# Performance work log

Hardware: AMD Instinct MI355X
Metric: run time of the kernel (lower is better)

The kernel has to match this reference:

```python
import jax, jax.numpy as jnp
import numpy as np

EMB = 1024
HEADS = 16
HEAD_DIM = EMB // HEADS


def setup_inputs() -> dict:
    key = jax.random.key(0)
    ks = jax.random.split(key, 12)
    B, S = 4, 2048
    scale = 1.0 / np.sqrt(EMB)
    inp = {
        'values': jax.random.normal(ks[0], (B, S, EMB), jnp.float32),
        'keys': jax.random.normal(ks[1], (B, S, EMB), jnp.float32),
        'query': jax.random.normal(ks[2], (B, S, EMB), jnp.float32),
        'Wv': jax.random.normal(ks[3], (EMB, EMB), jnp.float32) * scale,
        'bv': jnp.zeros((EMB,), jnp.float32),
        'Wk': jax.random.normal(ks[4], (EMB, EMB), jnp.float32) * scale,
        'bk': jnp.zeros((EMB,), jnp.float32),
        'Wq': jax.random.normal(ks[5], (EMB, EMB), jnp.float32) * scale,
        'bq': jnp.zeros((EMB,), jnp.float32),
        'Wo': jax.random.normal(ks[6], (EMB, EMB), jnp.float32) * scale,
        'bo': jnp.zeros((EMB,), jnp.float32),
    }
    return inp


def reference(values, keys, query, Wv, bv, Wk, bk, Wq, bq, Wo, bo):
    B, S, _ = values.shape
    # Linear projections (torch Linear: x @ W.T + b)
    v = values @ Wv.T + bv
    k = keys @ Wk.T + bk
    q = query @ Wq.T + bq
    # Reshape to (B, S, H, D) -- NOTE: original does NOT transpose heads,
    # so attention is computed across the HEAD axis per position.
    v = v.reshape(B, S, HEADS, HEAD_DIM)
    k = k.reshape(B, S, HEADS, HEAD_DIM)
    q = q.reshape(B, S, HEADS, HEAD_DIM)
    # (B,S,H,D) @ (B,S,D,H) -> (B,S,H,H) head-head scores
    scores = jnp.einsum('bshd,bsgd->bshg', q, k) * (HEAD_DIM ** -0.5)
    attn = jax.nn.softmax(scores, axis=-1)
    # (B,S,H,H) @ (B,S,H,D) -> (B,S,H,D)
    out = jnp.einsum('bshg,bsgd->bshd', attn, v)
    out = out.reshape(B, S, EMB)
    return out @ Wo.T + bo
```

## Files before the change

### kernel.cpp

```cpp
#include <hip/hip_runtime.h>
#include <stdint.h>

#define EMB 1024

typedef unsigned short u16;
typedef unsigned int u32;
typedef __attribute__((ext_vector_type(8))) unsigned short u16x8;
typedef __attribute__((ext_vector_type(8))) __bf16 bf16x8;
typedef __attribute__((ext_vector_type(4))) float f32x4;

__device__ __forceinline__ u16 f2bf(float f) {
  union { float f; uint32_t u; } x; x.f = f;
  uint32_t u = x.u;
  u += 0x7fff + ((u >> 16) & 1u);
  return (u16)(u >> 16);
}

__device__ __forceinline__ bf16x8 cvt8(float4 a, float4 b) {
  bf16x8 r;
  r[0] = (__bf16)a.x; r[1] = (__bf16)a.y; r[2] = (__bf16)a.z; r[3] = (__bf16)a.w;
  r[4] = (__bf16)b.x; r[5] = (__bf16)b.y; r[6] = (__bf16)b.z; r[7] = (__bf16)b.w;
  return r;
}

__device__ __forceinline__ void gl16(const u16* g, u16* l) {
  __builtin_amdgcn_global_load_lds(
      (const __attribute__((address_space(1))) void*)g,
      (__attribute__((address_space(3))) void*)l, 16, 0, 0);
}

__device__ __forceinline__ int xcd_logical(int orig, int nwg) {
  return (orig & 7) * (nwg >> 3) + (orig >> 3);
}

__global__ __launch_bounds__(256) void cvtw_kernel(
    const float* __restrict__ s0, u16* __restrict__ d0,
    const float* __restrict__ s1, u16* __restrict__ d1,
    const float* __restrict__ s2, u16* __restrict__ d2,
    const float* __restrict__ s3, u16* __restrict__ d3)
{
  const float* s; u16* d;
  switch (blockIdx.y) {
    case 0:  s = s0; d = d0; break;
    case 1:  s = s1; d = d1; break;
    case 2:  s = s2; d = d2; break;
    default: s = s3; d = d3; break;
  }
  const size_t i = (size_t)blockIdx.x * 256 + threadIdx.x;
  const float4* f = (const float4*)(s + i * 8);
  const float4 lo = f[0], hi = f[1];
  *(bf16x8*)(d + i * 8) = cvt8(lo, hi);
}

__global__ __launch_bounds__(256, 4) void qkv_fused_kernel(
    const float* __restrict__ Vx, const float* __restrict__ Kx,
    const float* __restrict__ Qx, const u16* __restrict__ Wb,
    const float* __restrict__ Bv, const float* __restrict__ Bk,
    const float* __restrict__ Bq,
    u16* __restrict__ cv, u16* __restrict__ ck, u16* __restrict__ cq,
    int N, int K, int M)
{
  __shared__ __attribute__((aligned(16))) u16 Al[2][128 * 32];
  __shared__ __attribute__((aligned(16))) u16 Bl[3][128 * 32];

  const int nwg = (N >> 7) * (M >> 7) * 3;
  const int logical = xcd_logical(blockIdx.x, nwg);
  const int per_z = (N >> 7) * (M >> 7);
  const int z = logical / per_z;
  const int rem = logical - z * per_z;
  const int nbx = N >> 7;
  const int by = rem / nbx, bx = rem - by * nbx;

  const float* X; const u16* W; const float* Bias; u16* C;
  switch (z) {
    case 0:  X = Vx; W = Wb;                   Bias = Bv; C = cv; break;
    case 1:  X = Kx; W = Wb + EMB * EMB;       Bias = Bk; C = ck; break;
    default: X = Qx; W = Wb + 2 * EMB * EMB;   Bias = Bq; C = cq; break;
  }

  const int tid  = threadIdx.x;
  const int lane = tid & 63;
  const int w    = tid >> 6;
  const int wm = w >> 1, wn = w & 1;
  const int r16 = lane & 15, quad = lane >> 4;
  const int bm = by * 128, bn = bx * 128;

  const int NSTEP = K >> 5;
  const int SM = NSTEP - 1;

  const int s0 = tid, s1 = tid + 256;
  const int r0 = s0 >> 2, c0 = s0 & 3;
  const int r1 = s1 >> 2, c1 = s1 & 3;
  const int lA0 = r0 * 32 + ((c0 ^ ((r0 >> 1) & 3)) * 8);
  const int lA1 = r1 * 32 + ((c1 ^ ((r1 >> 1) & 3)) * 8);
  const size_t xo0 = (size_t)(bm + r0) * K + c0 * 8;
  const size_t xo1 = (size_t)(bm + r1) * K + c1 * 8;

  const int bs0 = w * 64 + lane, bs1 = bs0 + 256;
  const int br0 = bs0 >> 2, bc0 = ((bs0 & 3) ^ ((br0 >> 1) & 3)) * 8;
  const int br1 = bs1 >> 2, bc1 = ((bs1 & 3) ^ ((br1 >> 1) & 3)) * 8;
  const u16* srcB0 = W + (size_t)(bn + br0) * K + bc0;
  const u16* srcB1 = W + (size_t)(bn + br1) * K + bc1;
  const int dB0o = (w * 64) * 8, dB1o = dB0o + 256 * 8;

  const int swz = (quad ^ ((r16 >> 1) & 3)) * 8;
  int offA[4], offB[4];
#pragma unroll
  for (int t = 0; t < 4; t++) {
    offA[t] = (wm * 64 + t * 16 + r16) * 32 + swz;
    offB[t] = (wn * 64 + t * 16 + r16) * 32 + swz;
  }

  f32x4 acc[4][4];
#pragma unroll
  for (int i = 0; i < 4; i++)
#pragma unroll
    for (int j = 0; j < 4; j++)
      acc[i][j] = f32x4{0.f, 0.f, 0.f, 0.f};

  float4 xa0 = *(const float4*)(X + xo0), xa1 = *(const float4*)(X + xo0 + 4);
  float4 xb0 = *(const float4*)(X + xo1), xb1 = *(const float4*)(X + xo1 + 4);
  gl16(srcB0, &Bl[0][dB0o]);
  gl16(srcB1, &Bl[0][dB1o]);
  gl16(srcB0 + 32, &Bl[1][dB0o]);
  gl16(srcB1 + 32, &Bl[1][dB1o]);
  *(bf16x8*)&Al[0][lA0] = cvt8(xa0, xa1);
  *(bf16x8*)&Al[0][lA1] = cvt8(xb0, xb1);
  xa0 = *(const float4*)(X + xo0 + 32); xa1 = *(const float4*)(X + xo0 + 36);
  xb0 = *(const float4*)(X + xo1 + 32); xb1 = *(const float4*)(X + xo1 + 36);
  asm volatile("s_waitcnt vmcnt(0) lgkmcnt(0)\n\ts_barrier" ::: "memory");

  int brd = 0;
  for (int it = 0; it < NSTEP; ++it) {
    const int acur = it & 1, anxt = acur ^ 1;
    const int bwr = (brd == 0) ? 2 : brd - 1;
    const int kn2 = ((it + 2) & SM) << 5;

    gl16(srcB0 + kn2, &Bl[bwr][dB0o]);
    gl16(srcB1 + kn2, &Bl[bwr][dB1o]);
    *(bf16x8*)&Al[anxt][lA0] = cvt8(xa0, xa1);
    *(bf16x8*)&Al[anxt][lA1] = cvt8(xb0, xb1);
    xa0 = *(const float4*)(X + xo0 + kn2); xa1 = *(const float4*)(X + xo0 + kn2 + 4);
    xb0 = *(const float4*)(X + xo1 + kn2); xb1 = *(const float4*)(X + xo1 + kn2 + 4);

    bf16x8 a[4], b[4];
#pragma unroll
    for (int t = 0; t < 4; t++) a[t] = *(const bf16x8*)&Al[acur][offA[t]];
#pragma unroll
    for (int t = 0; t < 4; t++) b[t] = *(const bf16x8*)&Bl[brd][offB[t]];

#pragma unroll
    for (int tm = 0; tm < 4; tm++)
#pragma unroll
      for (int tn = 0; tn < 4; tn++)
        acc[tm][tn] = __builtin_amdgcn_mfma_f32_16x16x32_bf16(a[tm], b[tn], acc[tm][tn], 0, 0, 0);

    asm volatile("s_waitcnt vmcnt(6) lgkmcnt(0)\n\ts_barrier" ::: "memory");
    brd = (brd == 2) ? 0 : brd + 1;
  }

#pragma unroll
  for (int tn = 0; tn < 4; tn++) {
    const int col = bn + wn * 64 + tn * 16 + r16;
    const float bias = Bias[col];
#pragma unroll
    for (int tm = 0; tm < 4; tm++) {
      const int row0 = bm + wm * 64 + tm * 16 + quad * 4;
#pragma unroll
      for (int r = 0; r < 4; r++)
        C[(size_t)(row0 + r) * N + col] = f2bf(acc[tm][tn][r] + bias);
    }
  }
}

__global__ __launch_bounds__(256, 4) void out_gemm_kernel(
    const u16* __restrict__ X, const u16* __restrict__ W,
    const float* __restrict__ Bias, float* __restrict__ C, int N, int K, int M)
{
  __shared__ __attribute__((aligned(16))) u16 Al[3][128 * 32];
  __shared__ __attribute__((aligned(16))) u16 Bl[3][64 * 32];

  const int nwg = (N >> 6) * (M >> 7);
  const int logical = xcd_logical(blockIdx.x, nwg);
  const int nbx = N >> 6;
  const int by = logical / nbx, bx = logical - by * nbx;

  const int tid  = threadIdx.x;
  const int lane = tid & 63;
  const int w    = tid >> 6;
  const int wm = w >> 1, wn = w & 1;
  const int r16 = lane & 15, quad = lane >> 4;
  const int bm = by * 128, bn = bx * 64;

  const int NSTEP = K >> 5;
  const int SM = NSTEP - 1;

  const int sA0 = w * 64 + lane, sA1 = sA0 + 256;
  const int rA0 = sA0 >> 2, cA0 = ((sA0 & 3) ^ ((rA0 >> 1) & 3)) * 8;
  const int rA1 = sA1 >> 2, cA1 = ((sA1 & 3) ^ ((rA1 >> 1) & 3)) * 8;
  const u16* srcA0 = X + (size_t)(bm + rA0) * K + cA0;
  const u16* srcA1 = X + (size_t)(bm + rA1) * K + cA1;
  const int dA0o = (w * 64) * 8, dA1o = dA0o + 256 * 8;

  const int sB = w * 64 + lane;
  const int rB = sB >> 2, cB = ((sB & 3) ^ ((rB >> 1) & 3)) * 8;
  const u16* srcB = W + (size_t)(bn + rB) * K + cB;
  const int dBo = (w * 64) * 8;

  const int swz = (quad ^ ((r16 >> 1) & 3)) * 8;
  int offA[4], offB[2];
#pragma unroll
  for (int t = 0; t < 4; t++)
    offA[t] = (wm * 64 + t * 16 + r16) * 32 + swz;
#pragma unroll
  for (int t = 0; t < 2; t++)
    offB[t] = (wn * 32 + t * 16 + r16) * 32 + swz;

  f32x4 acc[4][2];
#pragma unroll
  for (int i = 0; i < 4; i++)
#pragma unroll
    for (int j = 0; j < 2; j++)
      acc[i][j] = f32x4{0.f, 0.f, 0.f, 0.f};

  gl16(srcA0, &Al[0][dA0o]);
  gl16(srcA1, &Al[0][dA1o]);
  gl16(srcB,  &Bl[0][dBo]);
  gl16(srcA0 + 32, &Al[1][dA0o]);
  gl16(srcA1 + 32, &Al[1][dA1o]);
  gl16(srcB  + 32, &Bl[1][dBo]);
  asm volatile("s_waitcnt vmcnt(0)\n\ts_barrier" ::: "memory");

  int rd = 0;
  for (int it = 0; it < NSTEP; ++it) {
    const int wr = (rd == 0) ? 2 : rd - 1;
    const int kn2 = ((it + 2) & SM) << 5;

    gl16(srcA0 + kn2, &Al[wr][dA0o]);
    gl16(srcA1 + kn2, &Al[wr][dA1o]);
    gl16(srcB  + kn2, &Bl[wr][dBo]);

    bf16x8 a[4], b[2];
#pragma unroll
    for (int t = 0; t < 4; t++) a[t] = *(const bf16x8*)&Al[rd][offA[t]];
#pragma unroll
    for (int t = 0; t < 2; t++) b[t] = *(const bf16x8*)&Bl[rd][offB[t]];

#pragma unroll
    for (int tm = 0; tm < 4; tm++)
#pragma unroll
      for (int tn = 0; tn < 2; tn++)
        acc[tm][tn] = __builtin_amdgcn_mfma_f32_16x16x32_bf16(a[tm], b[tn], acc[tm][tn], 0, 0, 0);

    asm volatile("s_waitcnt vmcnt(3)\n\ts_barrier" ::: "memory");
    rd = (rd == 2) ? 0 : rd + 1;
  }

#pragma unroll
  for (int tn = 0; tn < 2; tn++) {
    const int col = bn + wn * 32 + tn * 16 + r16;
    const float bias = Bias[col];
#pragma unroll
    for (int tm = 0; tm < 4; tm++) {
      const int row0 = bm + wm * 64 + tm * 16 + quad * 4;
#pragma unroll
      for (int r = 0; r < 4; r++)
        C[(size_t)(row0 + r) * N + col] = acc[tm][tn][r] + bias;
    }
  }
}

__global__ __launch_bounds__(256, 5) void attn_heads_kernel(
    const u16* __restrict__ Q, const u16* __restrict__ Km,
    const u16* __restrict__ V, u16* __restrict__ O)
{
  const int tid = threadIdx.x, lane = tid & 63, w = tid >> 6;
  const int r16 = lane & 15, quad = lane >> 4;
  const size_t base = ((size_t)blockIdx.x * 4 + w) * EMB;

  u16 vb[4][8];
  const bool vload = quad < 2;
#pragma unroll
  for (int c = 0; c < 4; c++)
#pragma unroll
    for (int j = 0; j < 8; j++)
      vb[c][j] = vload ? V[base + (quad * 8 + j) * 64 + c * 16 + r16] : (u16)0;

  const bf16x8 ak0 = *(const bf16x8*)&Km[base + r16 * 64 + quad * 8];
  const bf16x8 ak1 = *(const bf16x8*)&Km[base + r16 * 64 + 32 + quad * 8];
  const bf16x8 bq0 = *(const bf16x8*)&Q[base + r16 * 64 + quad * 8];
  const bf16x8 bq1 = *(const bf16x8*)&Q[base + r16 * 64 + 32 + quad * 8];

  f32x4 s = f32x4{0.f, 0.f, 0.f, 0.f};
  s = __builtin_amdgcn_mfma_f32_16x16x32_bf16(ak0, bq0, s, 0, 0, 0);
  s = __builtin_amdgcn_mfma_f32_16x16x32_bf16(ak1, bq1, s, 0, 0, 0);

  float sv[4];
#pragma unroll
  for (int r = 0; r < 4; r++) sv[r] = s[r] * 0.125f;
  float m = fmaxf(fmaxf(sv[0], sv[1]), fmaxf(sv[2], sv[3]));
  m = fmaxf(m, __shfl_xor(m, 16));
  m = fmaxf(m, __shfl_xor(m, 32));
  float e[4];
  float sum = 0.f;
#pragma unroll
  for (int r = 0; r < 4; r++) { e[r] = __expf(sv[r] - m); sum += e[r]; }
  sum += __shfl_xor(sum, 16);
  sum += __shfl_xor(sum, 32);
  const float rs = 1.0f / sum;

  union { __bf16 h[2]; u32 u; } wlo, whi;
  wlo.h[0] = (__bf16)(e[0] * rs); wlo.h[1] = (__bf16)(e[1] * rs);
  whi.h[0] = (__bf16)(e[2] * rs); whi.h[1] = (__bf16)(e[3] * rs);

  const int src0 = r16 + quad * 32;
  const int src1 = src0 + 16;
  u32 a0 = (u32)__shfl((int)wlo.u, src0, 64);
  u32 a1 = (u32)__shfl((int)whi.u, src0, 64);
  u32 a2 = (u32)__shfl((int)wlo.u, src1, 64);
  u32 a3 = (u32)__shfl((int)whi.u, src1, 64);
  if (quad >= 2) { a0 = 0; a1 = 0; a2 = 0; a3 = 0; }
  union { u32 u[4]; bf16x8 v; } pa;
  pa.u[0] = a0; pa.u[1] = a1; pa.u[2] = a2; pa.u[3] = a3;

#pragma unroll
  for (int c = 0; c < 4; c++) {
    union { u16 s[8]; bf16x8 v; } vbv;
#pragma unroll
    for (int j = 0; j < 8; j++) vbv.s[j] = vb[c][j];
    f32x4 o = f32x4{0.f, 0.f, 0.f, 0.f};
    o = __builtin_amdgcn_mfma_f32_16x16x32_bf16(pa.v, vbv.v, o, 0, 0, 0);
#pragma unroll
    for (int r = 0; r < 4; r++)
      O[base + (size_t)(quad * 4 + r) * 64 + c * 16 + r16] = f2bf(o[r]);
  }
}

extern "C" void kernel_launch(void* const* d_in, const int* in_sizes, int n_in,
                              void* d_out, int out_size, void* d_ws, size_t ws_size,
                              hipStream_t stream)
{
  const float* values = (const float*)d_in[0];
  const float* keys   = (const float*)d_in[1];
  const float* query  = (const float*)d_in[2];
  const float* Wv = (const float*)d_in[3];
  const float* bv = (const float*)d_in[4];
  const float* Wk = (const float*)d_in[5];
  const float* bk = (const float*)d_in[6];
  const float* Wq = (const float*)d_in[7];
  const float* bq = (const float*)d_in[8];
  const float* Wo = (const float*)d_in[9];
  const float* bo = (const float*)d_in[10];

  const int M = in_sizes[0] / EMB;
  const int N = EMB, K = EMB;

  u16* q    = (u16*)d_ws;
  u16* kbuf = q + (size_t)M * EMB;
  u16* v    = (u16*)d_out;
  u16* wb   = v + (size_t)M * EMB;
  u16* ao   = q;

  const size_t base_ws = (size_t)2 * M * EMB * sizeof(u16);
  const bool wo_in_ws = ws_size >= base_ws + (size_t)EMB * EMB * sizeof(u16);
  u16* wob = wo_in_ws ? kbuf + (size_t)M * EMB : kbuf;

  dim3 blk(256, 1, 1);
  dim3 cwg(EMB * EMB / 8 / 256, wo_in_ws ? 4 : 3, 1);

  hipLaunchKernelGGL(cvtw_kernel, cwg, blk, 0, stream,
                     Wv, wb, Wk, wb + EMB * EMB, Wq, wb + 2 * EMB * EMB, Wo, wob);
  hipLaunchKernelGGL(qkv_fused_kernel, dim3((N / 128) * (M / 128) * 3, 1, 1), blk, 0, stream,
                     values, keys, query, wb, bv, bk, bq, v, kbuf, q, N, K, M);
  hipLaunchKernelGGL(attn_heads_kernel, dim3(M / 4, 1, 1), blk, 0, stream,
                     q, kbuf, v, ao);
  if (!wo_in_ws)
    hipLaunchKernelGGL(cvtw_kernel, dim3(EMB * EMB / 8 / 256, 1, 1), blk, 0, stream,
                       Wo, wob, (const float*)nullptr, (u16*)nullptr,
                       (const float*)nullptr, (u16*)nullptr,
                       (const float*)nullptr, (u16*)nullptr);
  hipLaunchKernelGGL(out_gemm_kernel, dim3((N / 64) * (M / 128), 1, 1), blk, 0, stream,
                     ao, wob, bo, (float*)d_out, N, K, M);
}
```

Measured before the change: 276.3 us.

## Enlarge QKV projection GEMM tiles to 256x256 with 8 waves and phased MFMA pipeline

Replaces the 128x128 QKV GEMM kernel with a 256x256 tile, 512-thread (8 wave) kernel using BK=64 double-buffered LDS, a new XOR swizzle, and four interleaved MFMA phases with setprio and barriers between global-to-LDS stores. The larger tile is meant to cut redundant global reads of the fp32 activations and bf16 weights and raise arithmetic intensity per byte loaded. In exchange it uses 128 KB of LDS per block, gives one block per CU, and launches far fewer workgroups (384), which risks lower occupancy and poorer latency hiding.

```diff
diff --git a/kernel.cpp b/kernel.cpp
--- a/kernel.cpp
+++ b/kernel.cpp
@@ -52,7 +52,7 @@
   *(bf16x8*)(d + i * 8) = cvt8(lo, hi);
 }
 
-__global__ __launch_bounds__(256, 4) void qkv_fused_kernel(
+__global__ __launch_bounds__(512, 2) void qkv256_kernel(
     const float* __restrict__ Vx, const float* __restrict__ Kx,
     const float* __restrict__ Qx, const u16* __restrict__ Wb,
     const float* __restrict__ Bv, const float* __restrict__ Bk,
@@ -60,15 +60,15 @@
     u16* __restrict__ cv, u16* __restrict__ ck, u16* __restrict__ cq,
     int N, int K, int M)
 {
-  __shared__ __attribute__((aligned(16))) u16 Al[2][128 * 32];
-  __shared__ __attribute__((aligned(16))) u16 Bl[3][128 * 32];
-
-  const int nwg = (N >> 7) * (M >> 7) * 3;
+  __shared__ __attribute__((aligned(16))) u16 Al[2][256 * 64];
+  __shared__ __attribute__((aligned(16))) u16 Bl[2][256 * 64];
+
+  const int per_z = (M >> 8) * (N >> 8);
+  const int nwg = per_z * 3;
   const int logical = xcd_logical(blockIdx.x, nwg);
-  const int per_z = (N >> 7) * (M >> 7);
   const int z = logical / per_z;
   const int rem = logical - z * per_z;
-  const int nbx = N >> 7;
+  const int nbx = N >> 8;
   const int by = rem / nbx, bx = rem - by * nbx;
 
   const float* X; const u16* W; const float* Bias; u16* C;
@@ -81,91 +81,114 @@
   const int tid  = threadIdx.x;
   const int lane = tid & 63;
   const int w    = tid >> 6;
-  const int wm = w >> 1, wn = w & 1;
+  const int wm = w >> 2, wn = w & 3;
   const int r16 = lane & 15, quad = lane >> 4;
-  const int bm = by * 128, bn = bx * 128;
-
-  const int NSTEP = K >> 5;
-  const int SM = NSTEP - 1;
-
-  const int s0 = tid, s1 = tid + 256;
-  const int r0 = s0 >> 2, c0 = s0 & 3;
-  const int r1 = s1 >> 2, c1 = s1 & 3;
-  const int lA0 = r0 * 32 + ((c0 ^ ((r0 >> 1) & 3)) * 8);
-  const int lA1 = r1 * 32 + ((c1 ^ ((r1 >> 1) & 3)) * 8);
-  const size_t xo0 = (size_t)(bm + r0) * K + c0 * 8;
-  const size_t xo1 = (size_t)(bm + r1) * K + c1 * 8;
-
-  const int bs0 = w * 64 + lane, bs1 = bs0 + 256;
-  const int br0 = bs0 >> 2, bc0 = ((bs0 & 3) ^ ((br0 >> 1) & 3)) * 8;
-  const int br1 = bs1 >> 2, bc1 = ((bs1 & 3) ^ ((br1 >> 1) & 3)) * 8;
-  const u16* srcB0 = W + (size_t)(bn + br0) * K + bc0;
-  const u16* srcB1 = W + (size_t)(bn + br1) * K + bc1;
-  const int dB0o = (w * 64) * 8, dB1o = dB0o + 256 * 8;
-
-  const int swz = (quad ^ ((r16 >> 1) & 3)) * 8;
-  int offA[4], offB[4];
-#pragma unroll
-  for (int t = 0; t < 4; t++) {
-    offA[t] = (wm * 64 + t * 16 + r16) * 32 + swz;
-    offB[t] = (wn * 64 + t * 16 + r16) * 32 + swz;
-  }
-
-  f32x4 acc[4][4];
-#pragma unroll
-  for (int i = 0; i < 4; i++)
+  const int bm = by * 256, bn = bx * 256;
+
+  const int prow = tid >> 3, pcol = tid & 7;
+  const int sw = ((pcol ^ (prow & 7)) * 8);
+  size_t xo[4]; int lA[4]; const u16* srcB[4]; int dB[4];
+#pragma unroll
+  for (int j = 0; j < 4; j++) {
+    const int row = prow + 64 * j;
+    xo[j]  = (size_t)(bm + row) * K + pcol * 8;
+    lA[j]  = row * 64 + sw;
+    srcB[j] = W + (size_t)(bn + row) * K + sw;
+    dB[j]  = (w * 64 + 512 * j) * 8;
+  }
+
+  const int swzr = r16 & 7;
+  const int slot0 = ((quad) ^ swzr) * 8;
+  const int slot1 = ((4 + quad) ^ swzr) * 8;
+  const int arow = wm * 128 + r16;
+  const int brow = wn * 64 + r16;
+
+  f32x4 acc[8][4];
+#pragma unroll
+  for (int i = 0; i < 8; i++)
 #pragma unroll
     for (int j = 0; j < 4; j++)
       acc[i][j] = f32x4{0.f, 0.f, 0.f, 0.f};
 
-  float4 xa0 = *(const float4*)(X + xo0), xa1 = *(const float4*)(X + xo0 + 4);
-  float4 xb0 = *(const float4*)(X + xo1), xb1 = *(const float4*)(X + xo1 + 4);
-  gl16(srcB0, &Bl[0][dB0o]);
-  gl16(srcB1, &Bl[0][dB1o]);
-  gl16(srcB0 + 32, &Bl[1][dB0o]);
-  gl16(srcB1 + 32, &Bl[1][dB1o]);
-  *(bf16x8*)&Al[0][lA0] = cvt8(xa0, xa1);
-  *(bf16x8*)&Al[0][lA1] = cvt8(xb0, xb1);
-  xa0 = *(const float4*)(X + xo0 + 32); xa1 = *(const float4*)(X + xo0 + 36);
-  xb0 = *(const float4*)(X + xo1 + 32); xb1 = *(const float4*)(X + xo1 + 36);
+  float4 x[8];
+#pragma unroll
+  for (int j = 0; j < 4; j++) gl16(srcB[j], &Bl[0][dB[j]]);
+#pragma unroll
+  for (int j = 0; j < 4; j++) {
+    x[2 * j]     = *(const float4*)(X + xo[j]);
+    x[2 * j + 1] = *(const float4*)(X + xo[j] + 4);
+  }
+#pragma unroll
+  for (int j = 0; j < 4; j++)
+    *(bf16x8*)&Al[0][lA[j]] = cvt8(x[2 * j], x[2 * j + 1]);
+#pragma unroll
+  for (int j = 0; j < 4; j++) {
+    x[2 * j]     = *(const float4*)(X + xo[j] + 64);
+    x[2 * j + 1] = *(const float4*)(X + xo[j] + 68);
+  }
   asm volatile("s_waitcnt vmcnt(0) lgkmcnt(0)\n\ts_barrier" ::: "memory");
 
-  int brd = 0;
-  for (int it = 0; it < NSTEP; ++it) {
-    const int acur = it & 1, anxt = acur ^ 1;
-    const int bwr = (brd == 0) ? 2 : brd - 1;
-    const int kn2 = ((it + 2) & SM) << 5;
-
-    gl16(srcB0 + kn2, &Bl[bwr][dB0o]);
-    gl16(srcB1 + kn2, &Bl[bwr][dB1o]);
-    *(bf16x8*)&Al[anxt][lA0] = cvt8(xa0, xa1);
-    *(bf16x8*)&Al[anxt][lA1] = cvt8(xb0, xb1);
-    xa0 = *(const float4*)(X + xo0 + kn2); xa1 = *(const float4*)(X + xo0 + kn2 + 4);
-    xb0 = *(const float4*)(X + xo1 + kn2); xb1 = *(const float4*)(X + xo1 + kn2 + 4);
-
-    bf16x8 a[4], b[4];
-#pragma unroll
-    for (int t = 0; t < 4; t++) a[t] = *(const bf16x8*)&Al[acur][offA[t]];
-#pragma unroll
-    for (int t = 0; t < 4; t++) b[t] = *(const bf16x8*)&Bl[brd][offB[t]];
-
-#pragma unroll
-    for (int tm = 0; tm < 4; tm++)
-#pragma unroll
-      for (int tn = 0; tn < 4; tn++)
-        acc[tm][tn] = __builtin_amdgcn_mfma_f32_16x16x32_bf16(a[tm], b[tn], acc[tm][tn], 0, 0, 0);
-
-    asm volatile("s_waitcnt vmcnt(6) lgkmcnt(0)\n\ts_barrier" ::: "memory");
-    brd = (brd == 2) ? 0 : brd + 1;
-  }
+#define PHASE_MFMA(KSLOT, H)                                                   \
+  {                                                                            \
+    bf16x8 a_[4], b_[4];                                                       \
+    _Pragma("unroll")                                                          \
+    for (int t4 = 0; t4 < 4; t4++)                                             \
+      a_[t4] = *(const bf16x8*)&Ac[(arow + ((H) * 4 + t4) * 16) * 64 + KSLOT]; \
+    _Pragma("unroll")                                                          \
+    for (int tn = 0; tn < 4; tn++)                                             \
+      b_[tn] = *(const bf16x8*)&Bc[(brow + tn * 16) * 64 + KSLOT];             \
+    __builtin_amdgcn_s_barrier();                                              \
+    __builtin_amdgcn_s_setprio(1);                                             \
+    _Pragma("unroll")                                                          \
+    for (int t4 = 0; t4 < 4; t4++)                                             \
+      _Pragma("unroll")                                                        \
+      for (int tn = 0; tn < 4; tn++)                                           \
+        acc[(H) * 4 + t4][tn] = __builtin_amdgcn_mfma_f32_16x16x32_bf16(       \
+            a_[t4], b_[tn], acc[(H) * 4 + t4][tn], 0, 0, 0);                   \
+    __builtin_amdgcn_s_setprio(0);                                             \
+  }
+
+  const int NT = K >> 6;
+  for (int t = 0; t < NT; ++t) {
+    const int cur = t & 1, nxt = cur ^ 1;
+    const int kn  = ((t + 1) & (NT - 1)) << 6;
+    const int kn2 = ((t + 2) & (NT - 1)) << 6;
+    const u16* Ac = Al[cur]; const u16* Bc = Bl[cur];
+    u16* An = Al[nxt];       u16* Bn = Bl[nxt];
+
+#pragma unroll
+    for (int j = 0; j < 4; j++) gl16(srcB[j] + kn, &Bn[dB[j]]);
+    __builtin_amdgcn_sched_barrier(0);
+    PHASE_MFMA(slot0, 0)
+    __builtin_amdgcn_s_barrier();
+
+    *(bf16x8*)&An[lA[0]] = cvt8(x[0], x[1]);
+    *(bf16x8*)&An[lA[1]] = cvt8(x[2], x[3]);
+    PHASE_MFMA(slot0, 1)
+    __builtin_amdgcn_s_barrier();
+
+    *(bf16x8*)&An[lA[2]] = cvt8(x[4], x[5]);
+    *(bf16x8*)&An[lA[3]] = cvt8(x[6], x[7]);
+    x[0] = *(const float4*)(X + xo[0] + kn2); x[1] = *(const float4*)(X + xo[0] + kn2 + 4);
+    x[2] = *(const float4*)(X + xo[1] + kn2); x[3] = *(const float4*)(X + xo[1] + kn2 + 4);
+    PHASE_MFMA(slot1, 0)
+    __builtin_amdgcn_s_barrier();
+
+    x[4] = *(const float4*)(X + xo[2] + kn2); x[5] = *(const float4*)(X + xo[2] + kn2 + 4);
+    x[6] = *(const float4*)(X + xo[3] + kn2); x[7] = *(const float4*)(X + xo[3] + kn2 + 4);
+    PHASE_MFMA(slot1, 1)
+    asm volatile("s_waitcnt vmcnt(8) lgkmcnt(0)" ::: "memory");
+    __builtin_amdgcn_s_barrier();
+  }
+#undef PHASE_MFMA
 
 #pragma unroll
   for (int tn = 0; tn < 4; tn++) {
     const int col = bn + wn * 64 + tn * 16 + r16;
     const float bias = Bias[col];
 #pragma unroll
-    for (int tm = 0; tm < 4; tm++) {
-      const int row0 = bm + wm * 64 + tm * 16 + quad * 4;
+    for (int tm = 0; tm < 8; tm++) {
+      const int row0 = bm + wm * 128 + tm * 16 + quad * 4;
 #pragma unroll
       for (int r = 0; r < 4; r++)
         C[(size_t)(row0 + r) * N + col] = f2bf(acc[tm][tn][r] + bias);
@@ -370,7 +393,8 @@
 
   hipLaunchKernelGGL(cvtw_kernel, cwg, blk, 0, stream,
                      Wv, wb, Wk, wb + EMB * EMB, Wq, wb + 2 * EMB * EMB, Wo, wob);
-  hipLaunchKernelGGL(qkv_fused_kernel, dim3((N / 128) * (M / 128) * 3, 1, 1), blk, 0, stream,
+  hipLaunchKernelGGL(qkv256_kernel, dim3((M / 256) * (N / 256) * 3, 1, 1),
+                     dim3(512, 1, 1), 0, stream,
                      values, keys, query, wb, bv, bk, bq, v, kbuf, q, N, K, M);
   hipLaunchKernelGGL(attn_heads_kernel, dim3(M / 4, 1, 1), blk, 0, stream,
                      q, kbuf, v, ao);
```

Result: slower. 284.1 us (+2.8%).
